# Performance work log

Measured on AMD Instinct MI355X. Metric: run time of the kernel, lower is better.

The kernel has to match this reference:

```python
import jax, jax.numpy as jnp
import numpy as np

B, S, D, H = 2, 2048, 1024, 16
DK = D // H  # 64

def setup_inputs() -> dict:
    key = jax.random.key(0)
    ks = jax.random.split(key, 12)
    scale = 1.0 / np.sqrt(D)
    return {
        "q": jax.random.normal(ks[0], (B, S, D), jnp.float32),
        "k": jax.random.normal(ks[1], (B, S, D), jnp.float32),
        "v": jax.random.normal(ks[2], (B, S, D), jnp.float32),
        "Wq": jax.random.normal(ks[3], (D, D), jnp.float32) * scale,
        "bq": jnp.zeros((D,), jnp.float32),
        "Wk": jax.random.normal(ks[4], (D, D), jnp.float32) * scale,
        "bk": jnp.zeros((D,), jnp.float32),
        "Wv": jax.random.normal(ks[5], (D, D), jnp.float32) * scale,
        "bv": jnp.zeros((D,), jnp.float32),
        "Wo": jax.random.normal(ks[6], (D, D), jnp.float32) * scale,
        "bo": jnp.zeros((D,), jnp.float32),
        "mask": jnp.ones((B, 1, S, S), jnp.bool_),
    }

def reference(q, k, v, Wq, bq, Wk, bk, Wv, bv, Wo, bo, mask):
    # Linear projections: y = x @ W^T + b (torch nn.Linear convention)
    def proj(x, W, b):
        return x @ W.T + b
    # [B,S,D] -> [B,H,S,DK]
    def split_heads(x):
        return x.reshape(B, S, H, DK).transpose(0, 2, 1, 3)

    query = split_heads(proj(q, Wq, bq))
    key_ = split_heads(proj(k, Wk, bk))
    value = split_heads(proj(v, Wv, bv))

    # NOTE: original uses out-of-place masked_fill whose result is discarded,
    # so mask has no effect on the computation (reproduced faithfully here).
    scores = jnp.einsum('bhqd,bhkd->bhqk', query, key_) / jnp.sqrt(
        jnp.asarray(DK, query.dtype))
    attn = jax.nn.softmax(scores, axis=-1)  # dropout p=0.0: identity
    x = jnp.einsum('bhqk,bhkd->bhqd', attn, value)
    x = x.transpose(0, 2, 1, 3).reshape(B, S, D)
    return proj(x, Wo, bo)
```

## Files before the change

### kernel.cpp

```cpp
#include <hip/hip_runtime.h>
#include <hip/hip_bf16.h>


typedef __attribute__((ext_vector_type(8))) short bf16x8;
typedef __attribute__((ext_vector_type(4))) float f32x4;
typedef unsigned short u16;
typedef unsigned int u32;

#define MFMA16(a, b, c) __builtin_amdgcn_mfma_f32_16x16x32_bf16(a, b, c, 0, 0, 0)
#define EXP2(x) __builtin_amdgcn_exp2f(x)

static __device__ __forceinline__ u16 f2bf(float f) {
    union { __hip_bfloat16 h; u16 u; } v;
    v.h = __float2bfloat16(f);
    return v.u;
}

static __device__ __forceinline__ u16 f2bf_fast(float f) {
    return (u16)((__float_as_uint(f) + 0x8000u) >> 16);
}

static __device__ __forceinline__ void gload16(const u16* g, u16* l) {
    __builtin_amdgcn_global_load_lds(
        (const __attribute__((address_space(1))) void*)g,
        (__attribute__((address_space(3))) void*)l, 16, 0, 0);
}

static __device__ __forceinline__ void cvt16(float4 f0, float4 f1,
                                             float4 f2, float4 f3, u16* o) {
    o[0]=f2bf(f0.x);  o[1]=f2bf(f0.y);  o[2]=f2bf(f0.z);  o[3]=f2bf(f0.w);
    o[4]=f2bf(f1.x);  o[5]=f2bf(f1.y);  o[6]=f2bf(f1.z);  o[7]=f2bf(f1.w);
    o[8]=f2bf(f2.x);  o[9]=f2bf(f2.y);  o[10]=f2bf(f2.z); o[11]=f2bf(f2.w);
    o[12]=f2bf(f3.x); o[13]=f2bf(f3.y); o[14]=f2bf(f3.z); o[15]=f2bf(f3.w);
}

struct CvtArgs16 { const float* in[16]; u16* out[16]; };

__global__ __launch_bounds__(256)
void cvt_multi(CvtArgs16 a)
{
    const int tsel = blockIdx.x >> 9;
    const int i = (((blockIdx.x & 511) * 256) + threadIdx.x) * 8;
    const float* in = a.in[tsel];
    u16* out = a.out[tsel];
    float4 x = *(const float4*)(in + i);
    float4 y = *(const float4*)(in + i + 4);
    u16 o[8];
    o[0]=f2bf(x.x); o[1]=f2bf(x.y); o[2]=f2bf(x.z); o[3]=f2bf(x.w);
    o[4]=f2bf(y.x); o[5]=f2bf(y.y); o[6]=f2bf(y.z); o[7]=f2bf(y.w);
    *(uint4*)(out + i) = *(uint4*)o;
}

struct GemmArgs {
    const float* F[3]; const u16* Wb[3]; const float* bias[3];
    u16* C[3]; float osc[3]; int epi[3];
};

__global__ __launch_bounds__(256)
void gemm_qkv(GemmArgs g)
{
    __shared__ u16 lds_f[2][128 * 40];
    __shared__ u16 lds_g[2][128 * 32];

    const int z = blockIdx.y;
    const float* Fp = g.F[z];
    const u16*  Gp = g.Wb[z];
    const int epi = g.epi[z];

    const int t    = threadIdx.x;
    const int lane = t & 63;
    const int w    = t >> 6;
    const int wm   = w >> 1, wn = w & 1;
    const int ll   = lane & 15;
    const int lg   = lane >> 4;

    const int bx  = blockIdx.x;
    const int swz = (bx & 7) * 32 + (bx >> 3);
    const int tile_m = (epi == 1 ? (swz & 7) : (swz >> 3)) * 128;
    const int tile_n = (epi == 1 ? (swz >> 3) : (swz & 7)) * 128;

    const int rowF = (epi == 1) ? tile_n : tile_m;
    const int rowG = (epi == 1) ? tile_m : tile_n;

    const int c0   = w * 2;
    const int lrow = lane >> 2;
    const int lcol = (lane & 3) * 8;

    const int srow = t >> 1;
    const int scol = (t & 1) * 16;
    const float* Fbase = Fp + (size_t)(rowF + srow) * 1024 + scol;
    const u16*   Gb0   = Gp + (size_t)(rowG + c0 * 16 + lrow) * 1024 + lcol;

    f32x4 acc[4][4] = {};

    const u16* fbaseA; const u16* fbaseB; int strA, strB; int selA;
    if (epi == 1) { selA = 0; strA = 32; strB = 40; }
    else          { selA = 1; strA = 40; strB = 32; }

    #define DO_MFMA(buf)                                                       \
    {                                                                          \
        const u16* bA = selA ? lds_f[buf] : lds_g[buf];                        \
        const u16* bB = selA ? lds_g[buf] : lds_f[buf];                        \
        bf16x8 af[4], bfr[4];                                                  \
        _Pragma("unroll")                                                      \
        for (int i = 0; i < 4; i++)                                            \
            af[i] = *(bf16x8*)&bA[(wm * 64 + i * 16 + ll) * strA + lg * 8];    \
        _Pragma("unroll")                                                      \
        for (int j = 0; j < 4; j++)                                            \
            bfr[j] = *(bf16x8*)&bB[(wn * 64 + j * 16 + ll) * strB + lg * 8];   \
        _Pragma("unroll")                                                      \
        for (int i = 0; i < 4; i++)                                            \
            _Pragma("unroll")                                                  \
            for (int j = 0; j < 4; j++)                                        \
                acc[i][j] = MFMA16(af[i], bfr[j], acc[i][j]);                  \
    }

    #define LOAD_F(dst0, dst1, dst2, dst3, s)                                  \
    {                                                                          \
        const float* Fs = Fbase + (s) * 32;                                    \
        dst0 = *(const float4*)(Fs);                                           \
        dst1 = *(const float4*)(Fs + 4);                                       \
        dst2 = *(const float4*)(Fs + 8);                                       \
        dst3 = *(const float4*)(Fs + 12);                                      \
    }

    #define WRITE_F(buf, s0, s1, s2, s3)                                       \
    {                                                                          \
        u16 tmp[16];                                                           \
        cvt16(s0, s1, s2, s3, tmp);                                            \
        *(uint4*)&lds_f[buf][srow * 40 + scol]     = *(uint4*)tmp;             \
        *(uint4*)&lds_f[buf][srow * 40 + scol + 8] = *(uint4*)(tmp + 8);       \
    }

    #define LOAD_G(buf, s)                                                     \
    {                                                                          \
        _Pragma("unroll")                                                      \
        for (int j = 0; j < 2; j++)                                            \
            gload16(Gb0 + (size_t)j * 16 * 1024 + (s) * 32,                    \
                    &lds_g[buf][(c0 + j) * 512]);                              \
    }

    float4 a0, a1, a2, a3, b0, b1, b2, b3;
    LOAD_G(0, 0);
    LOAD_F(a0, a1, a2, a3, 0);
    WRITE_F(0, a0, a1, a2, a3);
    LOAD_F(a0, a1, a2, a3, 1);
    __syncthreads();

    for (int it = 0; it < 16; ++it) {
        const int s0 = it * 2;
        if (s0 + 2 < 32) LOAD_F(b0, b1, b2, b3, s0 + 2);
        if (s0 + 1 < 32) LOAD_G(1, s0 + 1);
        DO_MFMA(0);
        if (s0 + 1 < 32) WRITE_F(1, a0, a1, a2, a3);
        __syncthreads();

        const int s1 = s0 + 1;
        if (s1 + 2 < 32) LOAD_F(a0, a1, a2, a3, s1 + 2);
        if (s1 + 1 < 32) LOAD_G(0, s1 + 1);
        if (s1 < 32) DO_MFMA(1);
        if (s1 + 1 < 32) WRITE_F(0, b0, b1, b2, b3);
        __syncthreads();
    }

    #undef DO_MFMA
    #undef LOAD_F
    #undef WRITE_F
    #undef LOAD_G

    const float osc = g.osc[z];
    const float* bias = g.bias[z];
    u16* Cp = g.C[z];

    #pragma unroll
    for (int i = 0; i < 4; i++) {
        const int row0 = tile_m + wm * 64 + i * 16 + lg * 4;
        #pragma unroll
        for (int j = 0; j < 4; j++) {
            const int col = tile_n + wn * 64 + j * 16 + ll;
            if (epi == 1) {
                const int b = col >> 11, s = col & 2047;
                #pragma unroll
                for (int r = 0; r < 4; r++)
                    Cp[(size_t)(b * 1024 + row0 + r) * 2048 + s] =
                        f2bf(acc[i][j][r] + bias[row0 + r]);
            } else {
                const float bias_v = bias[col];
                const int h = col >> 6, dk = col & 63;
                const int b = row0 >> 11;
                #pragma unroll
                for (int r = 0; r < 4; r++) {
                    const int s = (row0 + r) & 2047;
                    Cp[((size_t)(b * 16 + h) * 2048 + s) * 64 + dk] =
                        f2bf((acc[i][j][r] + bias_v) * osc);
                }
            }
        }
    }
}

__global__ __launch_bounds__(256)
void gemm_out(const u16* __restrict__ Ap, const u16* __restrict__ Wp,
              const float* __restrict__ bias, float* __restrict__ Cp)
{
    __shared__ u16 lds_a[2][128 * 32];
    __shared__ u16 lds_b[2][64 * 32];

    const int t    = threadIdx.x;
    const int lane = t & 63;
    const int w    = t >> 6;
    const int wm   = w >> 1, wn = w & 1;
    const int ll   = lane & 15;
    const int lg   = lane >> 4;

    const int bx  = blockIdx.x;
    const int swz = (bx & 7) * 64 + (bx >> 3);
    const int tile_m = (swz >> 4) * 128;
    const int tile_n = (swz & 15) * 64;

    const int lrow = lane >> 2;
    const int lcol = (lane & 3) * 8;

    f32x4 acc[4][2] = {};

    #define OSTAGE(buf, kt)                                                    \
    {                                                                          \
        _Pragma("unroll")                                                      \
        for (int j = 0; j < 3; j++) {                                          \
            const int c = w * 3 + j;                                           \
            if (c < 8) {                                                       \
                const int row = tile_m + c * 16 + lrow;                        \
                const int col = (kt) + lcol;                                   \
                const u16* ga = Ap + ((size_t)((row >> 11) * 16 + (col >> 6))  \
                                      * 2048 + (row & 2047)) * 64 + (col & 63);\
                gload16(ga, &lds_a[buf][c * 512]);                             \
            } else {                                                           \
                const int cc = c - 8;                                          \
                gload16(Wp + (size_t)(tile_n + cc * 16 + lrow) * 1024          \
                        + (kt) + lcol, &lds_b[buf][cc * 512]);                 \
            }                                                                  \
        }                                                                      \
    }

    OSTAGE(0, 0);
    __syncthreads();

    int cur = 0;
    for (int kt = 0; kt < 1024; kt += 32) {
        if (kt + 32 < 1024) OSTAGE(cur ^ 1, kt + 32);

        bf16x8 af[4], bfr[2];
        #pragma unroll
        for (int i = 0; i < 4; i++)
            af[i] = *(bf16x8*)&lds_a[cur][(wm * 64 + i * 16 + ll) * 32 + lg * 8];
        #pragma unroll
        for (int j = 0; j < 2; j++)
            bfr[j] = *(bf16x8*)&lds_b[cur][(wn * 32 + j * 16 + ll) * 32 + lg * 8];
        #pragma unroll
        for (int i = 0; i < 4; i++)
            #pragma unroll
            for (int j = 0; j < 2; j++)
                acc[i][j] = MFMA16(af[i], bfr[j], acc[i][j]);

        __syncthreads();
        cur ^= 1;
    }
    #undef OSTAGE

    #pragma unroll
    for (int i = 0; i < 4; i++) {
        const int row0 = tile_m + wm * 64 + i * 16 + lg * 4;
        #pragma unroll
        for (int j = 0; j < 2; j++) {
            const int col = tile_n + wn * 32 + j * 16 + ll;
            const float bias_v = bias[col];
            #pragma unroll
            for (int r = 0; r < 4; r++)
                Cp[(size_t)(row0 + r) * 1024 + col] = acc[i][j][r] + bias_v;
        }
    }
}

__global__ __launch_bounds__(512)
void attn_kernel(const u16* __restrict__ Qh, const u16* __restrict__ Kh,
                 const u16* __restrict__ Vt, u16* __restrict__ Oh)
{
    __shared__ u16 lds_k[2][64 * 64];
    __shared__ u16 lds_v[2][64 * 64];
    __shared__ u16 lds_p[8][16 * 64];

    const int t    = threadIdx.x;
    const int lane = t & 63;
    const int w    = t >> 6;
    const int ll   = lane & 15;
    const int lg   = lane >> 4;
    const int r7   = ll & 7;

    const int bx  = blockIdx.x;
    const int swz = (bx & 7) * 64 + (bx >> 3);
    const int qt = swz & 15;
    const int bh = swz >> 4;
    const int q0 = qt * 128 + w * 16;

    const u16* Qbase = Qh + ((size_t)bh * 2048 + q0 + ll) * 64 + lg * 8;
    const bf16x8 bq0 = *(const bf16x8*)(Qbase);
    const bf16x8 bq1 = *(const bf16x8*)(Qbase + 32);

    bf16x8 bones;
    #pragma unroll
    for (int i = 0; i < 8; i++) bones[i] = (short)0x3F80;

    f32x4 acc[4] = {};
    f32x4 acc_l = {};

    const int srow = lane >> 3;
    const int scol = 8 * ((lane & 7) ^ srow);
    const u16* Kg = Kh + (size_t)bh * 2048 * 64;
    const u16* Vg = Vt + (size_t)bh * 64 * 2048;

    #define ASTAGE(buf, kt)                                                    \
    {                                                                          \
        const int rr = w * 8 + srow;                                           \
        gload16(Kg + (size_t)((kt) + rr) * 64 + scol, &lds_k[buf][w * 512]);   \
        gload16(Vg + (size_t)rr * 2048 + (kt) + scol, &lds_v[buf][w * 512]);   \
    }

    ASTAGE(0, 0);
    __syncthreads();

    u16* lp = lds_p[w];
    int cur = 0;

    for (int kt = 0; kt < 2048; kt += 64) {
        if (kt + 64 < 2048) ASTAGE(cur ^ 1, kt + 64);

        f32x4 s[4];
        __builtin_amdgcn_s_setprio(1);
        #pragma unroll
        for (int ks = 0; ks < 4; ks++) {
            const u16* kp = &lds_k[cur][(ks * 16 + ll) * 64];
            const bf16x8 ak0 = *(const bf16x8*)(kp + ((lg * 8)      ^ (r7 * 8)));
            const bf16x8 ak1 = *(const bf16x8*)(kp + ((lg * 8 + 32) ^ (r7 * 8)));
            f32x4 z = {0.f, 0.f, 0.f, 0.f};
            z = MFMA16(ak0, bq0, z);
            z = MFMA16(ak1, bq1, z);
            s[ks] = z;
        }
        __builtin_amdgcn_s_setprio(0);

        #pragma unroll
        for (int ks = 0; ks < 4; ks++) {
            u16 pk[4];
            #pragma unroll
            for (int r = 0; r < 4; r++) pk[r] = f2bf_fast(EXP2(s[ks][r]));
            *(uint2*)&lp[ll * 64 + ((ks * 16 + lg * 4) ^ (r7 * 8))] = *(uint2*)pk;
        }

        __builtin_amdgcn_s_setprio(1);
        #pragma unroll
        for (int ks2 = 0; ks2 < 2; ks2++) {
            const int so = (ks2 * 32 + lg * 8) ^ (r7 * 8);
            const bf16x8 pa = *(const bf16x8*)&lp[ll * 64 + so];
            #pragma unroll
            for (int dt = 0; dt < 4; dt++) {
                const bf16x8 bv = *(const bf16x8*)&lds_v[cur][(dt * 16 + ll) * 64 + so];
                acc[dt] = MFMA16(pa, bv, acc[dt]);
            }
            acc_l = MFMA16(pa, bones, acc_l);
        }
        __builtin_amdgcn_s_setprio(0);

        __syncthreads();
        cur ^= 1;
    }
    #undef ASTAGE

    #pragma unroll
    for (int r = 0; r < 4; r++) {
        const float lq = 1.f / acc_l[r];
        const int qg = q0 + lg * 4 + r;
        u16* Op = Oh + ((size_t)bh * 2048 + qg) * 64 + ll;
        #pragma unroll
        for (int dt = 0; dt < 4; dt++)
            Op[dt * 16] = f2bf(acc[dt][r] * lq);
    }
}

extern "C" void kernel_launch(void* const* d_in, const int* in_sizes, int n_in,
                              void* d_out, int out_size, void* d_ws, size_t ws_size,
                              hipStream_t stream) {
    const float* q  = (const float*)d_in[0];
    const float* k  = (const float*)d_in[1];
    const float* v  = (const float*)d_in[2];
    const float* Wq = (const float*)d_in[3];
    const float* bq = (const float*)d_in[4];
    const float* Wk = (const float*)d_in[5];
    const float* bk = (const float*)d_in[6];
    const float* Wv = (const float*)d_in[7];
    const float* bv = (const float*)d_in[8];
    const float* Wo = (const float*)d_in[9];
    const float* bo = (const float*)d_in[10];
    float* out = (float*)d_out;

    const size_t M4 = (size_t)4 * 1024 * 1024;
    const size_t M1 = (size_t)1024 * 1024;
    const float qscale = 0.18033688011112042f;
    const dim3 blk(256);

    u16* Qh  = (u16*)d_ws;
    u16* Kh  = Qh + M4;
    u16* Vtb = Kh + M4;
    u16* Oh  = Vtb + M4;
    u16* Wqb = Oh + M4;
    u16* Wkb = Wqb + M1;
    u16* Wvb = Wkb + M1;
    u16* Wob = Wvb + M1;

    CvtArgs16 cv;
    for (int j = 0; j < 16; j++) { cv.in[j] = Wq; cv.out[j] = Wqb; }
    cv.in[0]=Wq; cv.out[0]=Wqb;
    cv.in[1]=Wk; cv.out[1]=Wkb;
    cv.in[2]=Wv; cv.out[2]=Wvb;
    cv.in[3]=Wo; cv.out[3]=Wob;
    cvt_multi<<<4 * 512, blk, 0, stream>>>(cv);

    GemmArgs ga;
    ga.F[0]=q;   ga.F[1]=k;   ga.F[2]=v;
    ga.Wb[0]=Wqb; ga.Wb[1]=Wkb; ga.Wb[2]=Wvb;
    ga.bias[0]=bq; ga.bias[1]=bk; ga.bias[2]=bv;
    ga.C[0]=Qh; ga.C[1]=Kh; ga.C[2]=Vtb;
    ga.osc[0]=qscale; ga.osc[1]=1.0f; ga.osc[2]=1.0f;
    ga.epi[0]=3; ga.epi[1]=3; ga.epi[2]=1;
    gemm_qkv<<<dim3(256, 3), blk, 0, stream>>>(ga);

    attn_kernel<<<512, dim3(512), 0, stream>>>(Qh, Kh, Vtb, Oh);

    gemm_out<<<512, blk, 0, stream>>>(Oh, Wob, bo, out);
}
```

Baseline: 138.5 us.

## Triple-buffer weight tiles in QKV GEMM with partial-wait barriers

Reworks the QKV projection GEMM main loop to use three LDS buffers for the bf16 weight tile, so async global-to-LDS loads run two k-steps ahead instead of one. It replaces __syncthreads with a custom barrier that waits only until at most two vector-memory ops are outstanding. It also drops the padded 40-element row stride for the fp32-converted activation tile in favour of a 32-element stride, which saves LDS but may bring back bank conflicts. The partial vmcnt wait depends on exact instruction counts and ordering to stay correct.

```diff
diff --git a/kernel.cpp b/kernel.cpp
--- a/kernel.cpp
+++ b/kernel.cpp
@@ -33,6 +33,13 @@
     o[8]=f2bf(f2.x);  o[9]=f2bf(f2.y);  o[10]=f2bf(f2.z); o[11]=f2bf(f2.w);
     o[12]=f2bf(f3.x); o[13]=f2bf(f3.y); o[14]=f2bf(f3.z); o[15]=f2bf(f3.w);
 }
+
+#define CBARRIER()                                                             \
+    do {                                                                       \
+        asm volatile("s_waitcnt vmcnt(2) lgkmcnt(0)" ::: "memory");            \
+        __builtin_amdgcn_sched_barrier(0);                                     \
+        __builtin_amdgcn_s_barrier();                                          \
+    } while (0)
 
 struct CvtArgs16 { const float* in[16]; u16* out[16]; };
 
@@ -59,8 +66,8 @@
 __global__ __launch_bounds__(256)
 void gemm_qkv(GemmArgs g)
 {
-    __shared__ u16 lds_f[2][128 * 40];
-    __shared__ u16 lds_g[2][128 * 32];
+    __shared__ u16 lds_f[2][128 * 32];
+    __shared__ u16 lds_g[3][128 * 32];
 
     const int z = blockIdx.y;
     const float* Fp = g.F[z];
@@ -92,22 +99,44 @@
     const u16*   Gb0   = Gp + (size_t)(rowG + c0 * 16 + lrow) * 1024 + lcol;
 
     f32x4 acc[4][4] = {};
-
-    const u16* fbaseA; const u16* fbaseB; int strA, strB; int selA;
-    if (epi == 1) { selA = 0; strA = 32; strB = 40; }
-    else          { selA = 1; strA = 40; strB = 32; }
-
-    #define DO_MFMA(buf)                                                       \
-    {                                                                          \
-        const u16* bA = selA ? lds_f[buf] : lds_g[buf];                        \
-        const u16* bB = selA ? lds_g[buf] : lds_f[buf];                        \
+    float4 f0, f1, f2, f3;
+
+    #define LOAD_F(s)                                                          \
+    {                                                                          \
+        const float* Fs = Fbase + (s) * 32;                                    \
+        f0 = *(const float4*)(Fs);                                             \
+        f1 = *(const float4*)(Fs + 4);                                         \
+        f2 = *(const float4*)(Fs + 8);                                         \
+        f3 = *(const float4*)(Fs + 12);                                        \
+    }
+
+    #define WRITE_F(buf)                                                       \
+    {                                                                          \
+        u16 tmp[16];                                                           \
+        cvt16(f0, f1, f2, f3, tmp);                                            \
+        *(uint4*)&lds_f[buf][srow * 32 + scol]     = *(uint4*)tmp;             \
+        *(uint4*)&lds_f[buf][srow * 32 + scol + 8] = *(uint4*)(tmp + 8);       \
+    }
+
+    #define LOAD_G(buf, s)                                                     \
+    {                                                                          \
+        _Pragma("unroll")                                                      \
+        for (int j = 0; j < 2; j++)                                            \
+            gload16(Gb0 + (size_t)j * 16 * 1024 + (s) * 32,                    \
+                    &lds_g[buf][(c0 + j) * 512]);                              \
+    }
+
+    #define DO_MFMA(gbuf, fbuf)                                                \
+    {                                                                          \
+        const u16* bA = (epi == 1) ? lds_g[gbuf] : lds_f[fbuf];                \
+        const u16* bB = (epi == 1) ? lds_f[fbuf] : lds_g[gbuf];                \
         bf16x8 af[4], bfr[4];                                                  \
         _Pragma("unroll")                                                      \
         for (int i = 0; i < 4; i++)                                            \
-            af[i] = *(bf16x8*)&bA[(wm * 64 + i * 16 + ll) * strA + lg * 8];    \
+            af[i] = *(bf16x8*)&bA[(wm * 64 + i * 16 + ll) * 32 + lg * 8];      \
         _Pragma("unroll")                                                      \
         for (int j = 0; j < 4; j++)                                            \
-            bfr[j] = *(bf16x8*)&bB[(wn * 64 + j * 16 + ll) * strB + lg * 8];   \
+            bfr[j] = *(bf16x8*)&bB[(wn * 64 + j * 16 + ll) * 32 + lg * 8];     \
         _Pragma("unroll")                                                      \
         for (int i = 0; i < 4; i++)                                            \
             _Pragma("unroll")                                                  \
@@ -115,58 +144,24 @@
                 acc[i][j] = MFMA16(af[i], bfr[j], acc[i][j]);                  \
     }
 
-    #define LOAD_F(dst0, dst1, dst2, dst3, s)                                  \
-    {                                                                          \
-        const float* Fs = Fbase + (s) * 32;                                    \
-        dst0 = *(const float4*)(Fs);                                           \
-        dst1 = *(const float4*)(Fs + 4);                                       \
-        dst2 = *(const float4*)(Fs + 8);                                       \
-        dst3 = *(const float4*)(Fs + 12);                                      \
-    }
-
-    #define WRITE_F(buf, s0, s1, s2, s3)                                       \
-    {                                                                          \
-        u16 tmp[16];                                                           \
-        cvt16(s0, s1, s2, s3, tmp);                                            \
-        *(uint4*)&lds_f[buf][srow * 40 + scol]     = *(uint4*)tmp;             \
-        *(uint4*)&lds_f[buf][srow * 40 + scol + 8] = *(uint4*)(tmp + 8);       \
-    }
-
-    #define LOAD_G(buf, s)                                                     \
-    {                                                                          \
-        _Pragma("unroll")                                                      \
-        for (int j = 0; j < 2; j++)                                            \
-            gload16(Gb0 + (size_t)j * 16 * 1024 + (s) * 32,                    \
-                    &lds_g[buf][(c0 + j) * 512]);                              \
-    }
-
-    float4 a0, a1, a2, a3, b0, b1, b2, b3;
+    LOAD_F(0);
     LOAD_G(0, 0);
-    LOAD_F(a0, a1, a2, a3, 0);
-    WRITE_F(0, a0, a1, a2, a3);
-    LOAD_F(a0, a1, a2, a3, 1);
-    __syncthreads();
-
-    for (int it = 0; it < 16; ++it) {
-        const int s0 = it * 2;
-        if (s0 + 2 < 32) LOAD_F(b0, b1, b2, b3, s0 + 2);
-        if (s0 + 1 < 32) LOAD_G(1, s0 + 1);
-        DO_MFMA(0);
-        if (s0 + 1 < 32) WRITE_F(1, a0, a1, a2, a3);
-        __syncthreads();
-
-        const int s1 = s0 + 1;
-        if (s1 + 2 < 32) LOAD_F(a0, a1, a2, a3, s1 + 2);
-        if (s1 + 1 < 32) LOAD_G(0, s1 + 1);
-        if (s1 < 32) DO_MFMA(1);
-        if (s1 + 1 < 32) WRITE_F(0, b0, b1, b2, b3);
-        __syncthreads();
-    }
-
-    #undef DO_MFMA
+    WRITE_F(0);
+    LOAD_G(1, 1);
+    CBARRIER();
+
+    for (int s = 0; s < 32; ++s) {
+        if (s + 1 < 32) LOAD_F(s + 1);
+        if (s + 2 < 32) LOAD_G((s + 2) % 3, s + 2);
+        DO_MFMA(s % 3, s & 1);
+        if (s + 1 < 32) WRITE_F((s + 1) & 1);
+        CBARRIER();
+    }
+
     #undef LOAD_F
     #undef WRITE_F
     #undef LOAD_G
+    #undef DO_MFMA
 
     const float osc = g.osc[z];
     const float* bias = g.bias[z];
```

Result: faster. 123.7 us (-10.7%).
